# Kernel tuning notes

Hardware: AMD Instinct MI355X
Metric: run time of the kernel (lower is better)

Reference implementation:

```python
import jax, jax.numpy as jnp
import numpy as np

# High-pass biquad coefficients from the original module
A_HP = (-1.99599, 0.996)
B_HP = (-2.0, 1.0)


def _biquad(x, b0, b1, a0, a1):
    """Direct-form-II-transposed biquad over time axis.
    x: [B, T]; coefficients are scalars; zero initial state (fresh buffers).
    """
    B = x.shape[0]
    init = (jnp.zeros((B,), x.dtype), jnp.zeros((B,), x.dtype))

    def step(mem, xi):  # xi: [B]
        m0, m1 = mem
        yi = xi + m0
        new_m0 = m1 + b0 * xi - a0 * yi
        new_m1 = b1 * xi - a1 * yi
        return (new_m0, new_m1), yi

    _, y = jax.lax.scan(step, init, x.T)  # scan over T
    return y.T  # [B, T]


def setup_inputs() -> dict:
    key = jax.random.key(0)
    kx, kn, k1, k2, k3, k4 = jax.random.split(key, 6)
    B, T = 4096, 16000
    x = jax.random.normal(kx, (B, T), dtype=jnp.float32)
    n = jax.random.normal(kn, (B, T), dtype=jnp.float32)
    # _rand_resp: 0.75 * (uniform[0,1) - 0.5), shape [batch]
    rr = lambda k: (0.75 * (jax.random.uniform(k, (B,), dtype=jnp.float32) - 0.5))
    return {"x": x, "n": n, "a_x": rr(k1), "b_x": rr(k2), "a_n": rr(k3), "b_n": rr(k4)}


def reference(x, n, a_x, b_x, a_n, b_n):
    # Signal path: fixed high-pass biquad, then random-response biquad.
    # NOTE (faithful to source): b[0], b[1] / a[0], a[1] index the BATCH-sized
    # random vectors, i.e. only the first two entries act as coefficients.
    x = _biquad(x, B_HP[0], B_HP[1], A_HP[0], A_HP[1])
    x = _biquad(x, b_x[0], b_x[1], a_x[0], a_x[1])
    n = _biquad(n, B_HP[0], B_HP[1], A_HP[0], A_HP[1])
    n = _biquad(n, b_n[0], b_n[1], a_n[0], a_n[1])
    return (x, n)
```

## Files before the change

kernel.cpp:

```cpp
#include <hip/hip_runtime.h>

#define T_LEN 16000
#define SEG_L 63
#define NSEG 254
#define ROWS 4096

#define HP_NA0  1.99599f
#define HP_NA1 -0.996f
#define HP_B0  -2.0f
#define HP_B1   1.0f

__device__ __forceinline__ void mm4(const float* A, const float* B, float* C) {
#pragma unroll
  for (int r = 0; r < 4; ++r) {
#pragma unroll
    for (int c = 0; c < 4; ++c) {
      float s = 0.f;
#pragma unroll
      for (int k = 0; k < 4; ++k) s = fmaf(A[r * 4 + k], B[k * 4 + c], s);
      C[r * 4 + c] = s;
    }
  }
}

__global__ void setup_kernel(const float* __restrict__ a_x, const float* __restrict__ b_x,
                             const float* __restrict__ a_n, const float* __restrict__ b_n,
                             float* __restrict__ ws) {
  int p = threadIdx.x;
  if (p >= 2) return;
  const float* a = p ? a_n : a_x;
  const float* b = p ? b_n : b_x;
  float a0 = a[0], a1 = a[1], b0 = b[0], b1 = b[1];

  float M[16] = {
      HP_NA0,   1.f, 0.f,  0.f,
      HP_NA1,   0.f, 0.f,  0.f,
      b0 - a0,  0.f, -a0,  1.f,
      b1 - a1,  0.f, -a1,  0.f};

  float cur[16], res[16], tmp[16];
#pragma unroll
  for (int i = 0; i < 16; ++i) { cur[i] = M[i]; res[i] = M[i]; }
  for (int s = 0; s < 5; ++s) {
    mm4(cur, cur, tmp);
#pragma unroll
    for (int i = 0; i < 16; ++i) cur[i] = tmp[i];
    mm4(res, cur, tmp);
#pragma unroll
    for (int i = 0; i < 16; ++i) res[i] = tmp[i];
  }
  float* dst = ws + p * 128;
#pragma unroll
  for (int i = 0; i < 16; ++i) dst[i] = res[i];
  for (int k = 1; k < 8; ++k) {
    mm4(res, res, tmp);
#pragma unroll
    for (int i = 0; i < 16; ++i) { res[i] = tmp[i]; dst[k * 16 + i] = res[i]; }
  }
}

__launch_bounds__(256)
__global__ void filt_kernel(const float* __restrict__ x, const float* __restrict__ n,
                            const float* __restrict__ a_x, const float* __restrict__ b_x,
                            const float* __restrict__ a_n, const float* __restrict__ b_n,
                            const float* __restrict__ ws, float* __restrict__ out) {
  __shared__ float buf[T_LEN];
  __shared__ float sd[NSEG * 5 + 2];
  __shared__ float Pm[128];

  const int bid = blockIdx.x;
  const int path = bid >> 12;
  const int row = bid & 4095;
  const int tid = threadIdx.x;

  const float* src = (path ? n : x) + (size_t)row * T_LEN;
  float* dst = out + (size_t)path * ((size_t)ROWS * T_LEN) + (size_t)row * T_LEN;

  const float4* s4 = reinterpret_cast<const float4*>(src);
  float4* b4 = reinterpret_cast<float4*>(buf);
  for (int i = tid; i < T_LEN / 4; i += 256) b4[i] = s4[i];
  if (tid < 128) Pm[tid] = ws[path * 128 + tid];

  const float* aa = path ? a_n : a_x;
  const float* bb = path ? b_n : b_x;
  const float a0r = aa[0], a1r = aa[1], b0r = bb[0], b1r = bb[1];
  const float na0r = -a0r, na1r = -a1r;
  __syncthreads();

  const int t = tid;

  float p0 = 0.f, p1 = 0.f, q0 = 0.f, q1 = 0.f;
  if (t < NSEG) {
    const int base = t * SEG_L;
    for (int j = 0; j < SEG_L; ++j) {
      const int idx = base + j;
      const float xv = (idx < T_LEN) ? buf[idx] : 0.f;
      const float y1 = xv + p0;
      const float np0 = fmaf(HP_NA0, y1, fmaf(HP_B0, xv, p1));
      p1 = fmaf(HP_NA1, y1, HP_B1 * xv);
      p0 = np0;
      const float y2 = y1 + q0;
      const float nq0 = fmaf(na0r, y2, fmaf(b0r, y1, q1));
      q1 = fmaf(na1r, y2, b1r * y1);
      q0 = nq0;
    }
    sd[t * 5 + 0] = p0; sd[t * 5 + 1] = p1; sd[t * 5 + 2] = q0; sd[t * 5 + 3] = q1;
  }
  __syncthreads();

  float d0 = p0, d1 = p1, d2 = q0, d3 = q1;
  for (int k = 0; k < 8; ++k) {
    const int o = 1 << k;
    float v0 = 0.f, v1 = 0.f, v2 = 0.f, v3 = 0.f;
    const bool act = (t < NSEG) && (t >= o);
    if (act) {
      v0 = sd[(t - o) * 5 + 0]; v1 = sd[(t - o) * 5 + 1];
      v2 = sd[(t - o) * 5 + 2]; v3 = sd[(t - o) * 5 + 3];
    }
    __syncthreads();
    if (act) {
      const float* P = Pm + k * 16;
      d0 = fmaf(P[0],  v0, fmaf(P[1],  v1, fmaf(P[2],  v2, fmaf(P[3],  v3, d0))));
      d1 = fmaf(P[4],  v0, fmaf(P[5],  v1, fmaf(P[6],  v2, fmaf(P[7],  v3, d1))));
      d2 = fmaf(P[8],  v0, fmaf(P[9],  v1, fmaf(P[10], v2, fmaf(P[11], v3, d2))));
      d3 = fmaf(P[12], v0, fmaf(P[13], v1, fmaf(P[14], v2, fmaf(P[15], v3, d3))));
      sd[t * 5 + 0] = d0; sd[t * 5 + 1] = d1; sd[t * 5 + 2] = d2; sd[t * 5 + 3] = d3;
    }
    __syncthreads();
  }

  if (t < NSEG) {
    float sp0 = 0.f, sp1 = 0.f, sq0 = 0.f, sq1 = 0.f;
    if (t > 0) {
      sp0 = sd[(t - 1) * 5 + 0]; sp1 = sd[(t - 1) * 5 + 1];
      sq0 = sd[(t - 1) * 5 + 2]; sq1 = sd[(t - 1) * 5 + 3];
    }
    const int base = t * SEG_L;
    const int lim = min(SEG_L, T_LEN - base);
    for (int j = 0; j < lim; ++j) {
      const int idx = base + j;
      const float xv = buf[idx];
      const float y1 = xv + sp0;
      const float np0 = fmaf(HP_NA0, y1, fmaf(HP_B0, xv, sp1));
      sp1 = fmaf(HP_NA1, y1, HP_B1 * xv);
      sp0 = np0;
      const float y2 = y1 + sq0;
      const float nq0 = fmaf(na0r, y2, fmaf(b0r, y1, sq1));
      sq1 = fmaf(na1r, y2, b1r * y1);
      sq0 = nq0;
      buf[idx] = y2;
    }
  }
  __syncthreads();

  float4* d4 = reinterpret_cast<float4*>(dst);
  for (int i = tid; i < T_LEN / 4; i += 256) d4[i] = b4[i];
}

extern "C" void kernel_launch(void* const* d_in, const int* in_sizes, int n_in,
                              void* d_out, int out_size, void* d_ws, size_t ws_size,
                              hipStream_t stream) {
  const float* x   = (const float*)d_in[0];
  const float* n   = (const float*)d_in[1];
  const float* a_x = (const float*)d_in[2];
  const float* b_x = (const float*)d_in[3];
  const float* a_n = (const float*)d_in[4];
  const float* b_n = (const float*)d_in[5];
  float* out = (float*)d_out;
  float* ws  = (float*)d_ws;

  hipLaunchKernelGGL(setup_kernel, dim3(1), dim3(64), 0, stream, a_x, b_x, a_n, b_n, ws);
  hipLaunchKernelGGL(filt_kernel, dim3(2 * ROWS), dim3(256), 0, stream,
                     x, n, a_x, b_x, a_n, b_n, ws, out);
}
```

Measured before the change: 965.4 us.

## Process each row in two halves with carried filter state to shrink LDS

Each block now handles its 16000-sample row in two 8000-sample halves, carrying the filter state from the end of the first half into the second. This cuts the LDS buffer from 64KB to about 32KB so more blocks can be resident per CU, and shortens the serial per-thread segments from 63 to 33 samples. The scan buffer is double-buffered as float4, which removes one barrier per step, and the setup kernel now forms M^33 by repeated multiplication. In exchange, the whole segmented scan runs twice per row with more barriers, and error accumulates differently.

```diff
diff --git a/kernel.cpp b/kernel.cpp
--- a/kernel.cpp
+++ b/kernel.cpp
@@ -1,9 +1,10 @@
 #include <hip/hip_runtime.h>
 
 #define T_LEN 16000
-#define SEG_L 63
-#define NSEG 254
-#define ROWS 4096
+#define HALF  8000
+#define SEG_L 33
+#define NSEG  243
+#define ROWS  4096
 
 #define HP_NA0  1.99599f
 #define HP_NA1 -0.996f
@@ -38,14 +39,11 @@
       b0 - a0,  0.f, -a0,  1.f,
       b1 - a1,  0.f, -a1,  0.f};
 
-  float cur[16], res[16], tmp[16];
+  float res[16], tmp[16];
 #pragma unroll
-  for (int i = 0; i < 16; ++i) { cur[i] = M[i]; res[i] = M[i]; }
-  for (int s = 0; s < 5; ++s) {
-    mm4(cur, cur, tmp);
-#pragma unroll
-    for (int i = 0; i < 16; ++i) cur[i] = tmp[i];
-    mm4(res, cur, tmp);
+  for (int i = 0; i < 16; ++i) res[i] = M[i];
+  for (int s = 1; s < SEG_L; ++s) {
+    mm4(res, M, tmp);
 #pragma unroll
     for (int i = 0; i < 16; ++i) res[i] = tmp[i];
   }
@@ -64,97 +62,112 @@
                             const float* __restrict__ a_x, const float* __restrict__ b_x,
                             const float* __restrict__ a_n, const float* __restrict__ b_n,
                             const float* __restrict__ ws, float* __restrict__ out) {
-  __shared__ float buf[T_LEN];
-  __shared__ float sd[NSEG * 5 + 2];
-  __shared__ float Pm[128];
+  __shared__ float  buf[HALF];
+  __shared__ float4 sd[2][NSEG];
+  __shared__ float  Pm[128];
+  __shared__ float  carry[4];
 
   const int bid = blockIdx.x;
   const int path = bid >> 12;
   const int row = bid & 4095;
-  const int tid = threadIdx.x;
+  const int t = threadIdx.x;
 
   const float* src = (path ? n : x) + (size_t)row * T_LEN;
   float* dst = out + (size_t)path * ((size_t)ROWS * T_LEN) + (size_t)row * T_LEN;
 
-  const float4* s4 = reinterpret_cast<const float4*>(src);
-  float4* b4 = reinterpret_cast<float4*>(buf);
-  for (int i = tid; i < T_LEN / 4; i += 256) b4[i] = s4[i];
-  if (tid < 128) Pm[tid] = ws[path * 128 + tid];
+  if (t < 128) Pm[t] = ws[path * 128 + t];
 
   const float* aa = path ? a_n : a_x;
   const float* bb = path ? b_n : b_x;
   const float a0r = aa[0], a1r = aa[1], b0r = bb[0], b1r = bb[1];
   const float na0r = -a0r, na1r = -a1r;
-  __syncthreads();
 
-  const int t = tid;
+  float i0 = 0.f, i1 = 0.f, i2 = 0.f, i3 = 0.f;
 
-  float p0 = 0.f, p1 = 0.f, q0 = 0.f, q1 = 0.f;
-  if (t < NSEG) {
-    const int base = t * SEG_L;
-    for (int j = 0; j < SEG_L; ++j) {
-      const int idx = base + j;
-      const float xv = (idx < T_LEN) ? buf[idx] : 0.f;
-      const float y1 = xv + p0;
-      const float np0 = fmaf(HP_NA0, y1, fmaf(HP_B0, xv, p1));
-      p1 = fmaf(HP_NA1, y1, HP_B1 * xv);
-      p0 = np0;
-      const float y2 = y1 + q0;
-      const float nq0 = fmaf(na0r, y2, fmaf(b0r, y1, q1));
-      q1 = fmaf(na1r, y2, b1r * y1);
-      q0 = nq0;
-    }
-    sd[t * 5 + 0] = p0; sd[t * 5 + 1] = p1; sd[t * 5 + 2] = q0; sd[t * 5 + 3] = q1;
-  }
-  __syncthreads();
+  for (int h = 0; h < 2; ++h) {
+    const float* hsrc = src + h * HALF;
 
-  float d0 = p0, d1 = p1, d2 = q0, d3 = q1;
-  for (int k = 0; k < 8; ++k) {
-    const int o = 1 << k;
-    float v0 = 0.f, v1 = 0.f, v2 = 0.f, v3 = 0.f;
-    const bool act = (t < NSEG) && (t >= o);
-    if (act) {
-      v0 = sd[(t - o) * 5 + 0]; v1 = sd[(t - o) * 5 + 1];
-      v2 = sd[(t - o) * 5 + 2]; v3 = sd[(t - o) * 5 + 3];
+    {
+      const float4* s4 = reinterpret_cast<const float4*>(hsrc);
+      float4* b4 = reinterpret_cast<float4*>(buf);
+      for (int i = t; i < HALF / 4; i += 256) b4[i] = s4[i];
     }
     __syncthreads();
-    if (act) {
-      const float* P = Pm + k * 16;
-      d0 = fmaf(P[0],  v0, fmaf(P[1],  v1, fmaf(P[2],  v2, fmaf(P[3],  v3, d0))));
-      d1 = fmaf(P[4],  v0, fmaf(P[5],  v1, fmaf(P[6],  v2, fmaf(P[7],  v3, d1))));
-      d2 = fmaf(P[8],  v0, fmaf(P[9],  v1, fmaf(P[10], v2, fmaf(P[11], v3, d2))));
-      d3 = fmaf(P[12], v0, fmaf(P[13], v1, fmaf(P[14], v2, fmaf(P[15], v3, d3))));
-      sd[t * 5 + 0] = d0; sd[t * 5 + 1] = d1; sd[t * 5 + 2] = d2; sd[t * 5 + 3] = d3;
+
+    float p0 = 0.f, p1 = 0.f, q0 = 0.f, q1 = 0.f;
+    if (t < NSEG) {
+      if (t == 0) { p0 = i0; p1 = i1; q0 = i2; q1 = i3; }
+      const int base = t * SEG_L;
+      for (int j = 0; j < SEG_L; ++j) {
+        const int idx = base + j;
+        const float xv = (idx < HALF) ? buf[idx] : 0.f;
+        const float y1 = xv + p0;
+        const float np0 = fmaf(HP_NA0, y1, fmaf(HP_B0, xv, p1));
+        p1 = fmaf(HP_NA1, y1, HP_B1 * xv);
+        p0 = np0;
+        const float y2 = y1 + q0;
+        const float nq0 = fmaf(na0r, y2, fmaf(b0r, y1, q1));
+        q1 = fmaf(na1r, y2, b1r * y1);
+        q0 = nq0;
+      }
+      sd[0][t] = make_float4(p0, p1, q0, q1);
     }
     __syncthreads();
+
+    float4 d = make_float4(p0, p1, q0, q1);
+    int cur = 0;
+    for (int k = 0; k < 8; ++k) {
+      const int o = 1 << k;
+      if (t < NSEG) {
+        if (t >= o) {
+          const float4 v = sd[cur][t - o];
+          const float* P = Pm + k * 16;
+          d.x = fmaf(P[0],  v.x, fmaf(P[1],  v.y, fmaf(P[2],  v.z, fmaf(P[3],  v.w, d.x))));
+          d.y = fmaf(P[4],  v.x, fmaf(P[5],  v.y, fmaf(P[6],  v.z, fmaf(P[7],  v.w, d.y))));
+          d.z = fmaf(P[8],  v.x, fmaf(P[9],  v.y, fmaf(P[10], v.z, fmaf(P[11], v.w, d.z))));
+          d.w = fmaf(P[12], v.x, fmaf(P[13], v.y, fmaf(P[14], v.z, fmaf(P[15], v.w, d.w))));
+        }
+        sd[cur ^ 1][t] = d;
+      }
+      cur ^= 1;
+      __syncthreads();
+    }
+
+    if (t < NSEG) {
+      float sp0 = i0, sp1 = i1, sq0 = i2, sq1 = i3;
+      if (t > 0) {
+        const float4 v = sd[0][t - 1];
+        sp0 = v.x; sp1 = v.y; sq0 = v.z; sq1 = v.w;
+      }
+      const int base = t * SEG_L;
+      const int lim = min(SEG_L, HALF - base);
+      for (int j = 0; j < lim; ++j) {
+        const int idx = base + j;
+        const float xv = buf[idx];
+        const float y1 = xv + sp0;
+        const float np0 = fmaf(HP_NA0, y1, fmaf(HP_B0, xv, sp1));
+        sp1 = fmaf(HP_NA1, y1, HP_B1 * xv);
+        sp0 = np0;
+        const float y2 = y1 + sq0;
+        const float nq0 = fmaf(na0r, y2, fmaf(b0r, y1, sq1));
+        sq1 = fmaf(na1r, y2, b1r * y1);
+        sq0 = nq0;
+        buf[idx] = y2;
+      }
+      if (t == NSEG - 1) {
+        carry[0] = sp0; carry[1] = sp1; carry[2] = sq0; carry[3] = sq1;
+      }
+    }
+    __syncthreads();
+
+    {
+      float4* d4 = reinterpret_cast<float4*>(dst) + h * (HALF / 4);
+      const float4* b4 = reinterpret_cast<const float4*>(buf);
+      for (int i = t; i < HALF / 4; i += 256) d4[i] = b4[i];
+    }
+    i0 = carry[0]; i1 = carry[1]; i2 = carry[2]; i3 = carry[3];
+    __syncthreads();
   }
-
-  if (t < NSEG) {
-    float sp0 = 0.f, sp1 = 0.f, sq0 = 0.f, sq1 = 0.f;
-    if (t > 0) {
-      sp0 = sd[(t - 1) * 5 + 0]; sp1 = sd[(t - 1) * 5 + 1];
-      sq0 = sd[(t - 1) * 5 + 2]; sq1 = sd[(t - 1) * 5 + 3];
-    }
-    const int base = t * SEG_L;
-    const int lim = min(SEG_L, T_LEN - base);
-    for (int j = 0; j < lim; ++j) {
-      const int idx = base + j;
-      const float xv = buf[idx];
-      const float y1 = xv + sp0;
-      const float np0 = fmaf(HP_NA0, y1, fmaf(HP_B0, xv, sp1));
-      sp1 = fmaf(HP_NA1, y1, HP_B1 * xv);
-      sp0 = np0;
-      const float y2 = y1 + sq0;
-      const float nq0 = fmaf(na0r, y2, fmaf(b0r, y1, sq1));
-      sq1 = fmaf(na1r, y2, b1r * y1);
-      sq0 = nq0;
-      buf[idx] = y2;
-    }
-  }
-  __syncthreads();
-
-  float4* d4 = reinterpret_cast<float4*>(dst);
-  for (int i = tid; i < T_LEN / 4; i += 256) d4[i] = b4[i];
 }
 
 extern "C" void kernel_launch(void* const* d_in, const int* in_sizes, int n_in,
```

Result: faster. 851.2 us (-11.8%).
